# Performance work log

Hardware: AMD Instinct MI355X
Metric: run time of the kernel (lower is better)

## Reference

```python
import jax, jax.numpy as jnp
import numpy as np

VOCAB, HIDDEN = 128, 1024
BATCH, SEQ = 64, 512


def setup_inputs() -> dict:
    key = jax.random.key(0)
    ks = jax.random.split(key, 6)
    scale = 1.0 / np.sqrt(HIDDEN)
    return {
        "x": jax.random.randint(ks[0], (BATCH, SEQ), 0, VOCAB, dtype=jnp.int32),
        "h": jnp.zeros((BATCH, HIDDEN), dtype=jnp.float32),
        "emb": jax.random.normal(ks[1], (VOCAB, HIDDEN), dtype=jnp.float32),
        "W_hx": jax.random.normal(ks[2], (HIDDEN, HIDDEN), dtype=jnp.float32) * scale,
        "b_hx": jnp.zeros((HIDDEN,), dtype=jnp.float32),
        "W_hh": jax.random.normal(ks[3], (HIDDEN, HIDDEN), dtype=jnp.float32) * scale,
        "W_out": jax.random.normal(ks[4], (HIDDEN, VOCAB), dtype=jnp.float32) * scale,
        "b_out": jnp.zeros((VOCAB,), dtype=jnp.float32),
    }


def reference(x, h, emb, W_hx, b_hx, W_hh, W_out, b_out):
    # x: [B, S] int indices; h: [B, H] initial hidden state
    x_emb = emb[x]  # [B, S, H] embedding lookup

    def step(h, xt):  # xt: [B, H]
        h_new = jnp.tanh(xt @ W_hx + b_hx + h @ W_hh)
        return h_new, h_new

    # scan over time axis (sequential dependency on h)
    h_final, hs = jax.lax.scan(step, h, jnp.swapaxes(x_emb, 0, 1))  # hs: [S, B, H]
    out = jnp.swapaxes(hs, 0, 1)  # [B, S, H]
    logits = out @ W_out + b_out  # [B, S, V]
    return logits, h_final
```

## Files before the change

### kernel.cpp

```cpp
#include <hip/hip_runtime.h>
#include <stdint.h>
#include <stddef.h>

#define VOCAB  128
#define HIDDEN 1024
#define BATCH  64
#define SEQ    512

#define NGROUP 4
#define BG     16
#define NWG    32
#define CJ     32
#define NVW    4
#define NTHR   512

#define POISON 0x7F800000u

#define E2_OFF   0
#define WOT_OFF  131072
#define BUF_OFF  196608

typedef __attribute__((ext_vector_type(8))) short short8_t;
typedef __attribute__((ext_vector_type(4))) float f32x4;

__device__ __forceinline__ uint4 cload4u(const void* p) {
    uint4 v;
    asm volatile("global_load_dwordx4 %0, %1, off sc0 sc1" : "=v"(v) : "v"(p));
    return v;
}
__device__ __forceinline__ void cstoreu(unsigned int* p, unsigned int x) {
    asm volatile("global_store_dword %0, %1, off sc0 sc1" :: "v"(p), "v"(x) : "memory");
}
#define WAITVM0() asm volatile("s_waitcnt vmcnt(0)" ::: "memory")
#define SCHED_FENCE() __builtin_amdgcn_sched_barrier(0)

__device__ __forceinline__ unsigned short bf16_rne(float f) {
    unsigned int u = __float_as_uint(f);
    u += 0x7FFF + ((u >> 16) & 1);
    return (unsigned short)(u >> 16);
}
__device__ __forceinline__ float bf16_f32(unsigned short h) {
    return __uint_as_float(((unsigned int)h) << 16);
}
__device__ __forceinline__ bool ok8(const uint4 a, const uint4 b) {
    return a.x != POISON && a.y != POISON && a.z != POISON && a.w != POISON
        && b.x != POISON && b.y != POISON && b.z != POISON && b.w != POISON;
}
__device__ __forceinline__ void unpack8(const uint4 a, const uint4 b,
                                        short8_t* h8, short8_t* l8) {
    (*h8)[0]=(short)(a.x>>16); (*l8)[0]=(short)(a.x&0xFFFF);
    (*h8)[1]=(short)(a.y>>16); (*l8)[1]=(short)(a.y&0xFFFF);
    (*h8)[2]=(short)(a.z>>16); (*l8)[2]=(short)(a.z&0xFFFF);
    (*h8)[3]=(short)(a.w>>16); (*l8)[3]=(short)(a.w&0xFFFF);
    (*h8)[4]=(short)(b.x>>16); (*l8)[4]=(short)(b.x&0xFFFF);
    (*h8)[5]=(short)(b.y>>16); (*l8)[5]=(short)(b.y&0xFFFF);
    (*h8)[6]=(short)(b.z>>16); (*l8)[6]=(short)(b.z&0xFFFF);
    (*h8)[7]=(short)(b.w>>16); (*l8)[7]=(short)(b.w&0xFFFF);
}

__global__ void e2_kernel(const float* __restrict__ emb, const float* __restrict__ W_hx,
                          const float* __restrict__ b_hx, float* __restrict__ E2) {
    int v = blockIdx.x >> 2;
    int j = (blockIdx.x & 3) * 256 + threadIdx.x;
    const float* er = emb + (size_t)v * HIDDEN;
    float acc = 0.f;
#pragma unroll 8
    for (int k = 0; k < HIDDEN; ++k)
        acc += er[k] * W_hx[(size_t)k * HIDDEN + j];
    E2[(size_t)v * HIDDEN + j] = acc + b_hx[j];
}

__global__ void wot_kernel(const float* __restrict__ W_out, unsigned short* __restrict__ WoT) {
    int v  = blockIdx.x;
    int k4 = threadIdx.x;
    ushort4 r;
    r.x = bf16_rne(W_out[(size_t)(k4*4+0)*VOCAB + v]);
    r.y = bf16_rne(W_out[(size_t)(k4*4+1)*VOCAB + v]);
    r.z = bf16_rne(W_out[(size_t)(k4*4+2)*VOCAB + v]);
    r.w = bf16_rne(W_out[(size_t)(k4*4+3)*VOCAB + v]);
    ((ushort4*)(WoT + (size_t)v * HIDDEN))[k4] = r;
}

__global__ void poison_kernel(unsigned int* __restrict__ bufs) {
    int i = blockIdx.x * 256 + threadIdx.x;
    ((uint4*)bufs)[i] = make_uint4(POISON, POISON, POISON, POISON);
}

extern "C" __global__ void __launch_bounds__(NTHR, 2)
rnn_kernel(const int* __restrict__ x, const float* __restrict__ h0,
           const float* __restrict__ W_hh,
           const float* __restrict__ E2, const unsigned short* __restrict__ WoT,
           const float* __restrict__ b_out,
           unsigned int* __restrict__ bufs,
           float* __restrict__ logits, float* __restrict__ hf) {
    extern __shared__ char lds_raw[];
    short* sHi   = (short*)lds_raw;
    short* sLo   = (short*)(lds_raw + 32768);
    float* sPart = (float*)(lds_raw + 65536);
    float* sPLog = (float*)(lds_raw + 81920);
    int*   sX    = (int*)(lds_raw + 83968);

    const int wg = blockIdx.x;
    const int g  = wg / NWG;
    const int w  = wg % NWG;
    const int b0 = g * BG;
    const int j0 = w * CJ;
    const int tid  = threadIdx.x;
    const int lane = tid & 63;
    const int wv   = tid >> 6;

    {
        const int4* xs4 = (const int4*)(x + (size_t)b0 * SEQ);
#pragma unroll
        for (int i = 0; i < 4; ++i)
            ((int4*)sX)[tid + 512 * i] = xs4[tid + 512 * i];
    }

    short8_t whi[2][4], wlo[2][4];
    {
        const int colb = lane & 15, kgrp = lane >> 4;
#pragma unroll
        for (int ct = 0; ct < 2; ++ct) {
            int col = j0 + ct * 16 + colb;
#pragma unroll
            for (int c = 0; c < 4; ++c) {
                int kb = wv * 128 + c * 32 + kgrp * 8;
#pragma unroll
                for (int e = 0; e < 8; ++e) {
                    float wval = W_hh[(size_t)(kb + e) * HIDDEN + col];
                    unsigned short hi = bf16_rne(wval);
                    whi[ct][c][e] = (short)hi;
                    wlo[ct][c][e] = (short)bf16_rne(wval - bf16_f32(hi));
                }
            }
        }
    }

    short8_t wvo[4];
    {
        const int colv = lane & 15, kgrp = lane >> 4;
#pragma unroll
        for (int c = 0; c < 4; ++c) {
            int kb = wv * 128 + c * 32 + kgrp * 8;
#pragma unroll
            for (int e = 0; e < 8; ++e)
                wvo[c][e] = (colv < NVW)
                    ? (short)WoT[(size_t)(w * NVW + colv) * HIDDEN + kb + e] : (short)0;
        }
    }
    const float boV = (tid < 64) ? b_out[w * NVW + (tid & 3)] : 0.f;
    __syncthreads();

    const int srow = tid >> 5;
    const int sslt = tid & 31;
    const int rb = tid >> 5, jb = tid & 31;
    const int ar = lane & 15, acg = lane >> 4;

    for (int t = 0; t < SEQ; ++t) {
        float e2p = E2[(size_t)sX[rb * SEQ + t] * HIDDEN + j0 + jb];

        if (t == 0) {
#pragma unroll
            for (int i = 0; i < 4; ++i) {
                int c = i * 32 + sslt;
                const float* p = h0 + (size_t)(b0 + srow) * HIDDEN + c * 8;
                short8_t h8, l8;
#pragma unroll
                for (int e = 0; e < 8; ++e) {
                    float vv = p[e];
                    unsigned short hi = bf16_rne(vv);
                    h8[e] = (short)hi;
                    l8[e] = (short)bf16_rne(vv - bf16_f32(hi));
                }
                int cs = (c ^ (srow & 7)) << 3;
                *(short8_t*)(sHi + srow * 1024 + cs) = h8;
                *(short8_t*)(sLo + srow * 1024 + cs) = l8;
            }
        } else {
            const unsigned int* src = bufs + ((size_t)((t - 1) & 3) << 16)
                                           + ((size_t)(b0 + srow) << 10);
            uint4 d[8];
            unsigned pend = 0xF;
            int guard = 0;
            do {
#pragma unroll
                for (int i = 0; i < 4; ++i)
                    if (pend & (1u << i)) {
                        int c = i * 32 + sslt;
                        d[2*i]   = cload4u(src + c * 8);
                        d[2*i+1] = cload4u(src + c * 8 + 4);
                    }
                WAITVM0();
                SCHED_FENCE();
                if ((pend & 1u) && ok8(d[0], d[1])) pend &= ~1u;
                if ((pend & 2u) && ok8(d[2], d[3])) pend &= ~2u;
                if ((pend & 4u) && ok8(d[4], d[5])) pend &= ~4u;
                if ((pend & 8u) && ok8(d[6], d[7])) pend &= ~8u;
                if (!pend) break;
                __builtin_amdgcn_s_sleep(1);
            } while (++guard < (1 << 20));
            SCHED_FENCE();
#pragma unroll
            for (int i = 0; i < 4; ++i) {
                int c = i * 32 + sslt;
                int cs = (c ^ (srow & 7)) << 3;
                short8_t h8, l8;
                unpack8(d[2*i], d[2*i+1], &h8, &l8);
                *(short8_t*)(sHi + srow * 1024 + cs) = h8;
                *(short8_t*)(sLo + srow * 1024 + cs) = l8;
            }
        }
        __syncthreads();

        f32x4 acc0 = {0.f, 0.f, 0.f, 0.f};
        f32x4 acc1 = {0.f, 0.f, 0.f, 0.f};
        f32x4 accL = {0.f, 0.f, 0.f, 0.f};
#pragma unroll
        for (int c = 0; c < 4; ++c) {
            int c8 = wv * 16 + c * 4 + acg;
            int off = ar * 1024 + ((c8 ^ (ar & 7)) << 3);
            short8_t ahi = *(const short8_t*)(sHi + off);
            short8_t alo = *(const short8_t*)(sLo + off);
            acc0 = __builtin_amdgcn_mfma_f32_16x16x32_bf16(ahi, whi[0][c], acc0, 0, 0, 0);
            acc1 = __builtin_amdgcn_mfma_f32_16x16x32_bf16(ahi, whi[1][c], acc1, 0, 0, 0);
            acc0 = __builtin_amdgcn_mfma_f32_16x16x32_bf16(alo, whi[0][c], acc0, 0, 0, 0);
            acc1 = __builtin_amdgcn_mfma_f32_16x16x32_bf16(alo, whi[1][c], acc1, 0, 0, 0);
            acc0 = __builtin_amdgcn_mfma_f32_16x16x32_bf16(ahi, wlo[0][c], acc0, 0, 0, 0);
            acc1 = __builtin_amdgcn_mfma_f32_16x16x32_bf16(ahi, wlo[1][c], acc1, 0, 0, 0);
            if (t > 0)
                accL = __builtin_amdgcn_mfma_f32_16x16x32_bf16(ahi, wvo[c], accL, 0, 0, 0);
        }
#pragma unroll
        for (int q = 0; q < 4; ++q) {
            sPart[wv * 512 + (acg * 4 + q) * 32 + ar]      = acc0[q];
            sPart[wv * 512 + (acg * 4 + q) * 32 + 16 + ar] = acc1[q];
        }
        if (t > 0 && ar < NVW) {
#pragma unroll
            for (int q = 0; q < 4; ++q)
                sPLog[wv * 64 + (acg * 4 + q) * 4 + ar] = accL[q];
        }
        __syncthreads();

        {
            float s = 0.f;
#pragma unroll
            for (int z = 0; z < 8; ++z) s += sPart[z * 512 + tid];
            float hn = tanhf(s + e2p);
            unsigned short hi = bf16_rne(hn);
            unsigned short lo = bf16_rne(hn - bf16_f32(hi));
            unsigned int pk = ((unsigned int)hi << 16) | (unsigned int)lo;
            size_t idx = ((size_t)(b0 + rb) << 10) + j0 + jb;
            cstoreu(bufs + ((size_t)(t & 3) << 16) + idx, pk);
            cstoreu(bufs + ((size_t)((t + 2) & 3) << 16) + idx, POISON);
            if (t == SEQ - 1)
                hf[(size_t)(b0 + rb) * HIDDEN + j0 + jb] = hn;
        }

        if (t > 0 && tid < 64) {
            int b = tid >> 2, v = tid & 3;
            float s = 0.f;
#pragma unroll
            for (int z = 0; z < 8; ++z) s += sPLog[z * 64 + b * 4 + v];
            logits[((size_t)(b0 + b) * SEQ + (t - 1)) * VOCAB + w * NVW + v] = s + boV;
        }
    }

    {
        const unsigned int* src = bufs + ((size_t)((SEQ - 1) & 3) << 16)
                                       + ((size_t)(b0 + srow) << 10);
        uint4 d[8];
        unsigned pend = 0xF;
        int guard = 0;
        do {
#pragma unroll
            for (int i = 0; i < 4; ++i)
                if (pend & (1u << i)) {
                    int c = i * 32 + sslt;
                    d[2*i]   = cload4u(src + c * 8);
                    d[2*i+1] = cload4u(src + c * 8 + 4);
                }
            WAITVM0();
            SCHED_FENCE();
            if ((pend & 1u) && ok8(d[0], d[1])) pend &= ~1u;
            if ((pend & 2u) && ok8(d[2], d[3])) pend &= ~2u;
            if ((pend & 4u) && ok8(d[4], d[5])) pend &= ~4u;
            if ((pend & 8u) && ok8(d[6], d[7])) pend &= ~8u;
            if (!pend) break;
            __builtin_amdgcn_s_sleep(1);
        } while (++guard < (1 << 20));
        SCHED_FENCE();
#pragma unroll
        for (int i = 0; i < 4; ++i) {
            int c = i * 32 + sslt;
            int cs = (c ^ (srow & 7)) << 3;
            short8_t h8, l8;
            unpack8(d[2*i], d[2*i+1], &h8, &l8);
            *(short8_t*)(sHi + srow * 1024 + cs) = h8;
        }
    }
    __syncthreads();
    {
        f32x4 accL = {0.f, 0.f, 0.f, 0.f};
#pragma unroll
        for (int c = 0; c < 4; ++c) {
            int c8 = wv * 16 + c * 4 + acg;
            int off = ar * 1024 + ((c8 ^ (ar & 7)) << 3);
            short8_t ahi = *(const short8_t*)(sHi + off);
            accL = __builtin_amdgcn_mfma_f32_16x16x32_bf16(ahi, wvo[c], accL, 0, 0, 0);
        }
        if (ar < NVW) {
#pragma unroll
            for (int q = 0; q < 4; ++q)
                sPLog[wv * 64 + (acg * 4 + q) * 4 + ar] = accL[q];
        }
        __syncthreads();
        if (tid < 64) {
            int b = tid >> 2, v = tid & 3;
            float s = 0.f;
#pragma unroll
            for (int z = 0; z < 8; ++z) s += sPLog[z * 64 + b * 4 + v];
            logits[((size_t)(b0 + b) * SEQ + (SEQ - 1)) * VOCAB + w * NVW + v] = s + boV;
        }
    }
}

extern "C" void kernel_launch(void* const* d_in, const int* in_sizes, int n_in,
                              void* d_out, int out_size, void* d_ws, size_t ws_size,
                              hipStream_t stream) {
    (void)in_sizes; (void)n_in; (void)out_size; (void)ws_size;
    const int*   x     = (const int*)  d_in[0];
    const float* h0    = (const float*)d_in[1];
    const float* emb   = (const float*)d_in[2];
    const float* W_hx  = (const float*)d_in[3];
    const float* b_hx  = (const float*)d_in[4];
    const float* W_hh  = (const float*)d_in[5];
    const float* W_out = (const float*)d_in[6];
    const float* b_out = (const float*)d_in[7];

    float* logits = (float*)d_out;
    float* hf     = logits + (size_t)BATCH * SEQ * VOCAB;

    float* ws  = (float*)d_ws;
    float* E2  = ws + E2_OFF;
    unsigned short* WoT = (unsigned short*)(ws + WOT_OFF);
    unsigned int*   bufs = (unsigned int*)(ws + BUF_OFF);

    poison_kernel<<<256, 256, 0, stream>>>(bufs);
    e2_kernel<<<512, 256, 0, stream>>>(emb, W_hx, b_hx, E2);
    wot_kernel<<<128, 256, 0, stream>>>(W_out, WoT);

    hipFuncSetAttribute(reinterpret_cast<const void*>(rnn_kernel),
                        hipFuncAttributeMaxDynamicSharedMemorySize, 116736);
    rnn_kernel<<<NGROUP * NWG, NTHR, 116736, stream>>>(x, h0, W_hh, E2, WoT, b_out,
                                                       bufs, logits, hf);
}
```

Before: 1.696 ms.

## Transpose hidden-state exchange layout so each wave loads its own slice, drop barrier

Stores the published hidden state batch-minor (column-major per group), so each wave polls and reads exactly the hidden columns its MFMA K-slice consumes. Each wave then writes only the LDS region it reads itself, which lets the kernel drop the __syncthreads between the exchange and the matmul. A barrier is added at the end of the step to protect shared buffers instead. The intent is to cut one block-wide barrier per timestep and shorten the dependency wait on the critical recurrent path. In exchange, global stores become strided per element and the packing logic is more involved.

```diff
diff --git a/kernel.cpp b/kernel.cpp
--- a/kernel.cpp
+++ b/kernel.cpp
@@ -42,20 +42,11 @@
 __device__ __forceinline__ float bf16_f32(unsigned short h) {
     return __uint_as_float(((unsigned int)h) << 16);
 }
-__device__ __forceinline__ bool ok8(const uint4 a, const uint4 b) {
-    return a.x != POISON && a.y != POISON && a.z != POISON && a.w != POISON
-        && b.x != POISON && b.y != POISON && b.z != POISON && b.w != POISON;
-}
-__device__ __forceinline__ void unpack8(const uint4 a, const uint4 b,
-                                        short8_t* h8, short8_t* l8) {
-    (*h8)[0]=(short)(a.x>>16); (*l8)[0]=(short)(a.x&0xFFFF);
-    (*h8)[1]=(short)(a.y>>16); (*l8)[1]=(short)(a.y&0xFFFF);
-    (*h8)[2]=(short)(a.z>>16); (*l8)[2]=(short)(a.z&0xFFFF);
-    (*h8)[3]=(short)(a.w>>16); (*l8)[3]=(short)(a.w&0xFFFF);
-    (*h8)[4]=(short)(b.x>>16); (*l8)[4]=(short)(b.x&0xFFFF);
-    (*h8)[5]=(short)(b.y>>16); (*l8)[5]=(short)(b.y&0xFFFF);
-    (*h8)[6]=(short)(b.z>>16); (*l8)[6]=(short)(b.z&0xFFFF);
-    (*h8)[7]=(short)(b.w>>16); (*l8)[7]=(short)(b.w&0xFFFF);
+__device__ __forceinline__ bool ok4(const uint4 v) {
+    return v.x != POISON && v.y != POISON && v.z != POISON && v.w != POISON;
+}
+__device__ __forceinline__ unsigned comp4(const uint4 v, int i) {
+    return i == 0 ? v.x : i == 1 ? v.y : i == 2 ? v.z : v.w;
 }
 
 __global__ void e2_kernel(const float* __restrict__ emb, const float* __restrict__ W_hx,
@@ -99,6 +90,8 @@
     float* sPart = (float*)(lds_raw + 65536);
     float* sPLog = (float*)(lds_raw + 81920);
     int*   sX    = (int*)(lds_raw + 83968);
+    unsigned* sHi32 = (unsigned*)sHi;
+    unsigned* sLo32 = (unsigned*)sLo;
 
     const int wg = blockIdx.x;
     const int g  = wg / NWG;
@@ -151,66 +144,57 @@
     const float boV = (tid < 64) ? b_out[w * NVW + (tid & 3)] : 0.f;
     __syncthreads();
 
-    const int srow = tid >> 5;
-    const int sslt = tid & 31;
     const int rb = tid >> 5, jb = tid & 31;
     const int ar = lane & 15, acg = lane >> 4;
+    const int cG = wv * 16 + (lane >> 2);
+    const int uBase = ((lane & 3));
 
     for (int t = 0; t < SEQ; ++t) {
         float e2p = E2[(size_t)sX[rb * SEQ + t] * HIDDEN + j0 + jb];
 
         if (t == 0) {
-#pragma unroll
-            for (int i = 0; i < 4; ++i) {
-                int c = i * 32 + sslt;
-                const float* p = h0 + (size_t)(b0 + srow) * HIDDEN + c * 8;
-                short8_t h8, l8;
-#pragma unroll
-                for (int e = 0; e < 8; ++e) {
-                    float vv = p[e];
-                    unsigned short hi = bf16_rne(vv);
-                    h8[e] = (short)hi;
-                    l8[e] = (short)bf16_rne(vv - bf16_f32(hi));
-                }
-                int cs = (c ^ (srow & 7)) << 3;
-                *(short8_t*)(sHi + srow * 1024 + cs) = h8;
-                *(short8_t*)(sLo + srow * 1024 + cs) = l8;
+            const float* hb = h0 + (size_t)b0 * HIDDEN + wv * 128 + lane * 2;
+#pragma unroll
+            for (int b = 0; b < 16; ++b) {
+                float2 f = *(const float2*)(hb + b * HIDDEN);
+                unsigned short h0s = bf16_rne(f.x);
+                unsigned short l0s = bf16_rne(f.x - bf16_f32(h0s));
+                unsigned short h1s = bf16_rne(f.y);
+                unsigned short l1s = bf16_rne(f.y - bf16_f32(h1s));
+                int u = b * 512 + ((cG ^ (b & 7)) << 2) + uBase;
+                sHi32[u] = (unsigned)h0s | ((unsigned)h1s << 16);
+                sLo32[u] = (unsigned)l0s | ((unsigned)l1s << 16);
             }
         } else {
             const unsigned int* src = bufs + ((size_t)((t - 1) & 3) << 16)
-                                           + ((size_t)(b0 + srow) << 10);
+                                           + ((size_t)g << 14) + (wv << 11) + (lane << 5);
             uint4 d[8];
-            unsigned pend = 0xF;
+            unsigned pend = 0xFFu;
             int guard = 0;
             do {
 #pragma unroll
-                for (int i = 0; i < 4; ++i)
-                    if (pend & (1u << i)) {
-                        int c = i * 32 + sslt;
-                        d[2*i]   = cload4u(src + c * 8);
-                        d[2*i+1] = cload4u(src + c * 8 + 4);
-                    }
+                for (int i = 0; i < 8; ++i)
+                    if (pend & (1u << i)) d[i] = cload4u(src + i * 4);
                 WAITVM0();
                 SCHED_FENCE();
-                if ((pend & 1u) && ok8(d[0], d[1])) pend &= ~1u;
-                if ((pend & 2u) && ok8(d[2], d[3])) pend &= ~2u;
-                if ((pend & 4u) && ok8(d[4], d[5])) pend &= ~4u;
-                if ((pend & 8u) && ok8(d[6], d[7])) pend &= ~8u;
+#pragma unroll
+                for (int i = 0; i < 8; ++i)
+                    if ((pend & (1u << i)) && ok4(d[i])) pend &= ~(1u << i);
                 if (!pend) break;
                 __builtin_amdgcn_s_sleep(1);
             } while (++guard < (1 << 20));
             SCHED_FENCE();
 #pragma unroll
-            for (int i = 0; i < 4; ++i) {
-                int c = i * 32 + sslt;
-                int cs = (c ^ (srow & 7)) << 3;
-                short8_t h8, l8;
-                unpack8(d[2*i], d[2*i+1], &h8, &l8);
-                *(short8_t*)(sHi + srow * 1024 + cs) = h8;
-                *(short8_t*)(sLo + srow * 1024 + cs) = l8;
+            for (int b = 0; b < 16; ++b) {
+                unsigned v0 = comp4(d[b >> 2], b & 3);
+                unsigned v1 = comp4(d[4 + (b >> 2)], b & 3);
+                unsigned hiP = (v0 >> 16) | (v1 & 0xFFFF0000u);
+                unsigned loP = (v0 & 0xFFFFu) | (v1 << 16);
+                int u = b * 512 + ((cG ^ (b & 7)) << 2) + uBase;
+                sHi32[u] = hiP;
+                sLo32[u] = loP;
             }
         }
-        __syncthreads();
 
         f32x4 acc0 = {0.f, 0.f, 0.f, 0.f};
         f32x4 acc1 = {0.f, 0.f, 0.f, 0.f};
@@ -250,7 +234,7 @@
             unsigned short hi = bf16_rne(hn);
             unsigned short lo = bf16_rne(hn - bf16_f32(hi));
             unsigned int pk = ((unsigned int)hi << 16) | (unsigned int)lo;
-            size_t idx = ((size_t)(b0 + rb) << 10) + j0 + jb;
+            size_t idx = ((size_t)g << 14) + (size_t)(j0 + jb) * 16 + rb;
             cstoreu(bufs + ((size_t)(t & 3) << 16) + idx, pk);
             cstoreu(bufs + ((size_t)((t + 2) & 3) << 16) + idx, POISON);
             if (t == SEQ - 1)
@@ -264,42 +248,37 @@
             for (int z = 0; z < 8; ++z) s += sPLog[z * 64 + b * 4 + v];
             logits[((size_t)(b0 + b) * SEQ + (t - 1)) * VOCAB + w * NVW + v] = s + boV;
         }
+        __syncthreads();
     }
 
     {
         const unsigned int* src = bufs + ((size_t)((SEQ - 1) & 3) << 16)
-                                       + ((size_t)(b0 + srow) << 10);
+                                       + ((size_t)g << 14) + (wv << 11) + (lane << 5);
         uint4 d[8];
-        unsigned pend = 0xF;
+        unsigned pend = 0xFFu;
         int guard = 0;
         do {
 #pragma unroll
-            for (int i = 0; i < 4; ++i)
-                if (pend & (1u << i)) {
-                    int c = i * 32 + sslt;
-                    d[2*i]   = cload4u(src + c * 8);
-                    d[2*i+1] = cload4u(src + c * 8 + 4);
-                }
+            for (int i = 0; i < 8; ++i)
+                if (pend & (1u << i)) d[i] = cload4u(src + i * 4);
             WAITVM0();
             SCHED_FENCE();
-            if ((pend & 1u) && ok8(d[0], d[1])) pend &= ~1u;
-            if ((pend & 2u) && ok8(d[2], d[3])) pend &= ~2u;
-            if ((pend & 4u) && ok8(d[4], d[5])) pend &= ~4u;
-            if ((pend & 8u) && ok8(d[6], d[7])) pend &= ~8u;
+#pragma unroll
+            for (int i = 0; i < 8; ++i)
+                if ((pend & (1u << i)) && ok4(d[i])) pend &= ~(1u << i);
             if (!pend) break;
             __builtin_amdgcn_s_sleep(1);
         } while (++guard < (1 << 20));
         SCHED_FENCE();
 #pragma unroll
-        for (int i = 0; i < 4; ++i) {
-            int c = i * 32 + sslt;
-            int cs = (c ^ (srow & 7)) << 3;
-            short8_t h8, l8;
-            unpack8(d[2*i], d[2*i+1], &h8, &l8);
-            *(short8_t*)(sHi + srow * 1024 + cs) = h8;
-        }
-    }
-    __syncthreads();
+        for (int b = 0; b < 16; ++b) {
+            unsigned v0 = comp4(d[b >> 2], b & 3);
+            unsigned v1 = comp4(d[4 + (b >> 2)], b & 3);
+            unsigned hiP = (v0 >> 16) | (v1 & 0xFFFF0000u);
+            int u = b * 512 + ((cG ^ (b & 7)) << 2) + uBase;
+            sHi32[u] = hiP;
+        }
+    }
     {
         f32x4 accL = {0.f, 0.f, 0.f, 0.f};
 #pragma unroll
```

Result: slower. 3.190 ms (+88.1%).
